# Performance work log

Measured on AMD Instinct MI355X. Metric: run time of the kernel, lower is better.

## Reference

```python
import jax, jax.numpy as jnp
import numpy as np

# Module constants derived from init_kwargs
XYZ_MIN = np.array([-40.0, -40.0, -1.0], dtype=np.float32)
XYZ_MAX = np.array([40.0, 40.0, 5.4], dtype=np.float32)
STEPSIZE = 0.5
VOX = (200, 200, 16)
NUM_VOXELS = VOX[0] * VOX[1] * VOX[2]
VOXEL_SIZE = float((np.prod(XYZ_MAX - XYZ_MIN) / NUM_VOXELS) ** (1.0 / 3.0))  # = 0.4
N_SAMPLES = int(np.linalg.norm(np.array([VOX[0] // 2, VOX[1] // 2, VOX[2] // 2]) + 1) / STEPSIZE) + 1  # 287


def setup_inputs() -> dict:
    key = jax.random.key(0)
    k1, k2, k3 = jax.random.split(key, 3)
    rays_o = jax.random.uniform(k1, (6, 90, 160, 3), dtype=jnp.float32)   # camera origins near scene center
    rays_d = jax.random.normal(k2, (6, 90, 160, 3), dtype=jnp.float32)    # ray directions
    voxel = jax.random.normal(k3, (1, 200, 200, 16), dtype=jnp.float32)   # density grid (C=1, X, Y, Z)
    return {"rays_o": rays_o, "rays_d": rays_d, "voxel": voxel}


def trilinear_sample(grid, pts):
    """align_corners=True trilinear interpolation.
    grid: (C, Dx, Dy, Dz) laid out as (world-x, world-y, world-z) axes
    pts:  (M, 3) world coords. Out-of-range pts are clamped (they are masked later).
    Returns (C, M).
    """
    xyz_min = jnp.asarray(XYZ_MIN)
    xyz_max = jnp.asarray(XYZ_MAX)
    sizes = jnp.asarray(np.array(grid.shape[1:], dtype=np.float32))
    u = (pts - xyz_min) / (xyz_max - xyz_min)              # normalized [0,1]
    idx = jnp.clip(u * (sizes - 1.0), 0.0, sizes - 1.0)    # voxel-space coords
    i0 = jnp.clip(jnp.floor(idx), 0.0, sizes - 2.0).astype(jnp.int32)
    f = idx - i0.astype(idx.dtype)                          # fractional offsets
    x0, y0, z0 = i0[:, 0], i0[:, 1], i0[:, 2]
    fx, fy, fz = f[:, 0], f[:, 1], f[:, 2]
    out = jnp.zeros((grid.shape[0], pts.shape[0]), dtype=grid.dtype)
    for dx in (0, 1):
        wx = fx if dx else (1.0 - fx)
        for dy in (0, 1):
            wy = fy if dy else (1.0 - fy)
            for dz in (0, 1):
                wz = fz if dz else (1.0 - fz)
                corner = grid[:, x0 + dx, y0 + dy, z0 + dz]   # (C, M) gather
                out = out + corner * (wx * wy * wz)[None, :]
    return out


def reference(rays_o, rays_d, voxel):
    xyz_min = jnp.asarray(XYZ_MIN)
    xyz_max = jnp.asarray(XYZ_MAX)
    ro = rays_o.reshape(-1, 3)                                # (M, 3)
    rd = rays_d.reshape(-1, 3)                                # (M, 3)
    # eval-mode sampling: deterministic Zval shared by all rays
    zval = STEPSIZE * VOXEL_SIZE * jnp.arange(N_SAMPLES, dtype=jnp.float32)  # (N,)
    pts = ro[:, None, :] + rd[:, None, :] * zval[None, :, None]             # (M, N, 3)
    mask_out = jnp.any((pts < xyz_min) | (pts > xyz_max), axis=-1)          # (M, N)
    density = trilinear_sample(voxel, pts.reshape(-1, 3))                   # (1, M*N)
    density = density.reshape(pts.shape[0], N_SAMPLES)                      # (M, N)
    # alpha compositing (render_type='density')
    delta = zval[-1] - zval[-2]                                             # constant step length
    alpha = jnp.where(mask_out, 0.0, 1.0 - jnp.exp(-jax.nn.softplus(density) * delta))
    trans = jnp.cumprod(jnp.clip(1.0 - alpha, 1e-10, None), axis=-1)        # (M, N)
    alphainv_cum = jnp.concatenate([jnp.ones_like(trans[:, :1]), trans], axis=-1)
    weights = alpha * alphainv_cum[:, :-1]                                  # (M, N)
    depth = jnp.sum(weights * zval[None, :], axis=-1)                       # (M,)
    return depth
```

## Files before the change

kernel.cpp:

```cpp
#include <hip/hip_runtime.h>
#include <math.h>

#define N_RAYS 86400
#define N_SAMP 287
#define GRP_W  16
#define N_CHUNK 18
#define LOG2E 1.4426950408889634f

#define ROW_SHR_OLD1(x, N)                                                   \
    __int_as_float(__builtin_amdgcn_update_dpp(                              \
        0x3f800000 , __float_as_int(x), 0x110 | (N), 0xF, 0xF, false))

#define SWZ(x, pat) __int_as_float(__builtin_amdgcn_ds_swizzle(__float_as_int(x), (pat)))
#define SWZ_BCAST15 0x1F0
#define SWZ_XOR(m)  (((m) << 10) | 0x1F)

struct F2 { float lo, hi; };

__global__ __launch_bounds__(256) void nerf_depth_kernel(
    const float* __restrict__ rays_o,
    const float* __restrict__ rays_d,
    const float* __restrict__ voxel,
    float* __restrict__ depth_out,
    float stepf, float delta)
{
    const int lane = threadIdx.x & 63;
    const int sub  = lane & (GRP_W - 1);
    const int grp  = lane >> 4;
    const int wave = (blockIdx.x * blockDim.x + threadIdx.x) >> 6;
    const int ray  = wave * 4 + grp;

    const float ox = rays_o[3*ray+0], oy = rays_o[3*ray+1], oz = rays_o[3*ray+2];
    const float dx = rays_d[3*ray+0], dy = rays_d[3*ray+1], dz = rays_d[3*ray+2];

    const float cx1 = 199.0f / 80.0f;                  const float cx0 = 40.0f * cx1;
    const float cz1 = 15.0f / (5.4f - (-1.0f));        const float cz0 = 1.0f * cz1;
    const float negdelta = -delta;

    float T = 1.0f;
    float depth_acc = 0.0f;
    bool  done = false;

    for (int c = 0; c < N_CHUNK; ++c) {
        const int  s     = c * GRP_W + sub;
        const bool valid = (s < N_SAMP);
        const float z  = __fmul_rn(stepf, (float)s);
        const float px = __fadd_rn(ox, __fmul_rn(dx, z));
        const float py = __fadd_rn(oy, __fmul_rn(dy, z));
        const float pz = __fadd_rn(oz, __fmul_rn(dz, z));
        const bool inside = !((fmaxf(fabsf(px), fabsf(py)) > 40.0f) |
                              (pz < -1.0f) | (pz > 5.4f));
        const bool inb = (!done) && valid && inside;

        const unsigned long long bal = __ballot(inb);
        if (((unsigned)(bal >> (grp * GRP_W)) & 0xFFFFu) == 0u) done = true;
        if (__all(done)) break;

        float alpha = 0.0f, az = 0.0f;
        if (inb) {
            float ix = fminf(fmaxf(__builtin_fmaf(px, cx1, cx0), 0.0f), 199.0f);
            float iy = fminf(fmaxf(__builtin_fmaf(py, cx1, cx0), 0.0f), 199.0f);
            float iz = fminf(fmaxf(__builtin_fmaf(pz, cz1, cz0), 0.0f), 15.0f);
            int x0 = min((int)ix, 198);
            int y0 = min((int)iy, 198);
            int z0 = min((int)iz, 14);
            float fx = ix - (float)x0;
            float fy = iy - (float)y0;
            float fz = iz - (float)z0;
            const float* p00 = voxel + ((x0 * 200 + y0) * 16 + z0);
            F2 q00, q01, q10, q11;
            __builtin_memcpy(&q00, p00,        8);
            __builtin_memcpy(&q01, p00 + 16,   8);
            __builtin_memcpy(&q10, p00 + 3200, 8);
            __builtin_memcpy(&q11, p00 + 3216, 8);
            float c00 = q00.lo + fz * (q00.hi - q00.lo);
            float c01 = q01.lo + fz * (q01.hi - q01.lo);
            float c10 = q10.lo + fz * (q10.hi - q10.lo);
            float c11 = q11.lo + fz * (q11.hi - q11.lo);
            float c0  = c00 + fy * (c01 - c00);
            float c1  = c10 + fy * (c11 - c10);
            float d   = c0  + fx * (c1  - c0);
            float e2 = exp2f(d * LOG2E);
            float lg = __log2f(1.0f + e2);
            alpha = 1.0f - exp2f(negdelta * lg);
            az = alpha * z;
        }

        float g = fmaxf(1.0f - alpha, 1e-10f);

        float P = g;
        P *= ROW_SHR_OLD1(P, 1);
        P *= ROW_SHR_OLD1(P, 2);
        P *= ROW_SHR_OLD1(P, 4);
        P *= ROW_SHR_OLD1(P, 8);
        float E = ROW_SHR_OLD1(P, 1);

        depth_acc = __builtin_fmaf(az, T * E, depth_acc);
        T *= SWZ(P, SWZ_BCAST15);

        if (T < 1e-6f) done = true;
    }

    depth_acc += SWZ(depth_acc, SWZ_XOR(1));
    depth_acc += SWZ(depth_acc, SWZ_XOR(2));
    depth_acc += SWZ(depth_acc, SWZ_XOR(4));
    depth_acc += SWZ(depth_acc, SWZ_XOR(8));
    if (sub == 0) depth_out[ray] = depth_acc;
}

extern "C" void kernel_launch(void* const* d_in, const int* in_sizes, int n_in,
                              void* d_out, int out_size, void* d_ws, size_t ws_size,
                              hipStream_t stream) {
    (void)in_sizes; (void)n_in; (void)d_ws; (void)ws_size; (void)out_size;
    const float* rays_o = (const float*)d_in[0];
    const float* rays_d = (const float*)d_in[1];
    const float* voxel  = (const float*)d_in[2];
    float* out = (float*)d_out;

    float rngz  = 5.4f - (-1.0f);
    float prod  = (80.0f * 80.0f) * rngz;
    float ratio = prod / 640000.0f;
    float stepf = (float)(0.5 * pow((double)ratio, 1.0 / 3.0));
    float delta = stepf * 286.0f - stepf * 285.0f;

    nerf_depth_kernel<<<N_RAYS / 16, 256, 0, stream>>>(rays_o, rays_d, voxel, out, stepf, delta);
}
```

Baseline: 26.91 us.

## Sort rays by analytic chunk count to balance wavefront work

Adds two pre-pass kernels. The first computes each ray's exit sample analytically from a ray/box intersection and builds a histogram of chunk counts. The second counting-sorts the rays by that count so rays of similar length share a wavefront, and the main kernel loops only up to each ray's chunk count instead of using a per-chunk ballot. This targets divergence and idle lanes from mixed ray lengths, at the cost of a memset, two extra launches, and scattered ray and output accesses.

```diff
diff --git a/kernel.cpp b/kernel.cpp
--- a/kernel.cpp
+++ b/kernel.cpp
@@ -17,18 +17,80 @@
 
 struct F2 { float lo, hi; };
 
+__device__ __forceinline__ int ray_nch(float ox, float oy, float oz,
+                                       float dx, float dy, float dz,
+                                       float stepf) {
+    float invx = 1.0f / __fmul_rn(dx, stepf);
+    float invy = 1.0f / __fmul_rn(dy, stepf);
+    float invz = 1.0f / __fmul_rn(dz, stepf);
+    float tx = fmaxf((40.0f - ox) * invx, (-40.0f - ox) * invx);
+    float ty = fmaxf((40.0f - oy) * invy, (-40.0f - oy) * invy);
+    float tz = fmaxf((5.4f - oz) * invz, (-1.0f - oz) * invz);
+    float te = fminf(fminf(fminf(tx, ty), tz), 300.0f);
+    int s_stop = min((int)te + 2, N_SAMP);
+    return (s_stop + GRP_W - 1) >> 4;
+}
+
+__global__ __launch_bounds__(256) void k_len(
+    const float* __restrict__ ro, const float* __restrict__ rd,
+    int* __restrict__ nch_arr, int* __restrict__ hist, float stepf)
+{
+    __shared__ int lh[N_CHUNK];
+    if (threadIdx.x < N_CHUNK) lh[threadIdx.x] = 0;
+    __syncthreads();
+    int t = blockIdx.x * 256 + threadIdx.x;
+    if (t < N_RAYS) {
+        int nch = ray_nch(ro[3*t], ro[3*t+1], ro[3*t+2],
+                          rd[3*t], rd[3*t+1], rd[3*t+2], stepf);
+        nch_arr[t] = nch;
+        atomicAdd(&lh[N_CHUNK - nch], 1);
+    }
+    __syncthreads();
+    if (threadIdx.x < N_CHUNK && lh[threadIdx.x])
+        atomicAdd(&hist[threadIdx.x], lh[threadIdx.x]);
+}
+
+__global__ __launch_bounds__(256) void k_scatter(
+    const int* __restrict__ nch_arr, const int* __restrict__ hist,
+    int* __restrict__ cursor, unsigned* __restrict__ sorted)
+{
+    __shared__ int lcount[N_CHUNK], lbase[N_CHUNK];
+    if (threadIdx.x < N_CHUNK) lcount[threadIdx.x] = 0;
+    __syncthreads();
+    int t = blockIdx.x * 256 + threadIdx.x;
+    int b = 0, rank = 0, nch = 0;
+    if (t < N_RAYS) {
+        nch = nch_arr[t];
+        b = N_CHUNK - nch;
+        rank = atomicAdd(&lcount[b], 1);
+    }
+    __syncthreads();
+    if (threadIdx.x < N_CHUNK && lcount[threadIdx.x])
+        lbase[threadIdx.x] = atomicAdd(&cursor[threadIdx.x], lcount[threadIdx.x]);
+    __syncthreads();
+    if (t < N_RAYS) {
+        int off = 0;
+        #pragma unroll
+        for (int i = 0; i < N_CHUNK; ++i) off += (i < b) ? hist[i] : 0;
+        sorted[off + lbase[b] + rank] = (unsigned)t | ((unsigned)nch << 20);
+    }
+}
+
 __global__ __launch_bounds__(256) void nerf_depth_kernel(
     const float* __restrict__ rays_o,
     const float* __restrict__ rays_d,
     const float* __restrict__ voxel,
+    const unsigned* __restrict__ sorted,
     float* __restrict__ depth_out,
     float stepf, float delta)
 {
     const int lane = threadIdx.x & 63;
     const int sub  = lane & (GRP_W - 1);
-    const int grp  = lane >> 4;
-    const int wave = (blockIdx.x * blockDim.x + threadIdx.x) >> 6;
-    const int ray  = wave * 4 + grp;
+    const int g    = (blockIdx.x * blockDim.x + threadIdx.x) >> 4;
+
+    const unsigned e = sorted[g];
+    const int ray = e & 0xFFFFF;
+    const int nch = e >> 20;
 
     const float ox = rays_o[3*ray+0], oy = rays_o[3*ray+1], oz = rays_o[3*ray+2];
     const float dx = rays_d[3*ray+0], dy = rays_d[3*ray+1], dz = rays_d[3*ray+2];
@@ -39,9 +101,10 @@
 
     float T = 1.0f;
     float depth_acc = 0.0f;
-    bool  done = false;
+    bool  dead = false;
 
-    for (int c = 0; c < N_CHUNK; ++c) {
+    int c = 0;
+    while (true) {
         const int  s     = c * GRP_W + sub;
         const bool valid = (s < N_SAMP);
         const float z  = __fmul_rn(stepf, (float)s);
@@ -50,11 +113,7 @@
         const float pz = __fadd_rn(oz, __fmul_rn(dz, z));
         const bool inside = !((fmaxf(fabsf(px), fabsf(py)) > 40.0f) |
                               (pz < -1.0f) | (pz > 5.4f));
-        const bool inb = (!done) && valid && inside;
-
-        const unsigned long long bal = __ballot(inb);
-        if (((unsigned)(bal >> (grp * GRP_W)) & 0xFFFFu) == 0u) done = true;
-        if (__all(done)) break;
+        const bool inb = inside && valid && !dead;
 
         float alpha = 0.0f, az = 0.0f;
         if (inb) {
@@ -86,9 +145,9 @@
             az = alpha * z;
         }
 
-        float g = fmaxf(1.0f - alpha, 1e-10f);
+        float gg = fmaxf(1.0f - alpha, 1e-10f);
 
-        float P = g;
+        float P = gg;
         P *= ROW_SHR_OLD1(P, 1);
         P *= ROW_SHR_OLD1(P, 2);
         P *= ROW_SHR_OLD1(P, 4);
@@ -98,7 +157,9 @@
         depth_acc = __builtin_fmaf(az, T * E, depth_acc);
         T *= SWZ(P, SWZ_BCAST15);
 
-        if (T < 1e-6f) done = true;
+        ++c;
+        dead = dead | (c >= nch) | (T < 1e-6f);
+        if (__all(dead)) break;
     }
 
     depth_acc += SWZ(depth_acc, SWZ_XOR(1));
@@ -111,11 +172,16 @@
 extern "C" void kernel_launch(void* const* d_in, const int* in_sizes, int n_in,
                               void* d_out, int out_size, void* d_ws, size_t ws_size,
                               hipStream_t stream) {
-    (void)in_sizes; (void)n_in; (void)d_ws; (void)ws_size; (void)out_size;
+    (void)in_sizes; (void)n_in; (void)ws_size; (void)out_size;
     const float* rays_o = (const float*)d_in[0];
     const float* rays_d = (const float*)d_in[1];
     const float* voxel  = (const float*)d_in[2];
     float* out = (float*)d_out;
+
+    int*      hist    = (int*)d_ws;
+    int*      cursor  = (int*)d_ws + 32;
+    int*      nch_arr = (int*)d_ws + 1024;
+    unsigned* sorted  = (unsigned*)((int*)d_ws + 1024 + N_RAYS);
 
     float rngz  = 5.4f - (-1.0f);
     float prod  = (80.0f * 80.0f) * rngz;
@@ -123,5 +189,10 @@
     float stepf = (float)(0.5 * pow((double)ratio, 1.0 / 3.0));
     float delta = stepf * 286.0f - stepf * 285.0f;
 
-    nerf_depth_kernel<<<N_RAYS / 16, 256, 0, stream>>>(rays_o, rays_d, voxel, out, stepf, delta);
+    hipMemsetAsync(d_ws, 0, 256, stream);
+    const int pb = (N_RAYS + 255) / 256;
+    k_len    <<<pb, 256, 0, stream>>>(rays_o, rays_d, nch_arr, hist, stepf);
+    k_scatter<<<pb, 256, 0, stream>>>(nch_arr, hist, cursor, sorted);
+    nerf_depth_kernel<<<N_RAYS / 16, 256, 0, stream>>>(rays_o, rays_d, voxel,
+                                                       sorted, out, stepf, delta);
 }
```

Result: slower. 38.92 us (+44.6%).

## Reformulate depth as telescoping transmittance sum and precompute ray exit chunk

Applied to the files above, without the earlier changes.

Rewrites depth compositing algebraically: instead of accumulating alpha*z*T per sample, it accumulates the inclusive transmittance prefix and recovers depth as stepf*(sum - 16*C*U). The per-chunk ballot is replaced by an analytic ray/box exit computation, and the gather/interpolation runs unconditionally with masking done by a select. Swizzles are replaced with DPP quad-perm and row-rotate reductions. Together these aim to cut cross-lane latency and divergence. In exchange, out-of-box lanes now issue loads and transcendentals, the 1e-10 clamp is dropped, and the telescoped form may round differently.

```diff
diff --git a/kernel.cpp b/kernel.cpp
--- a/kernel.cpp
+++ b/kernel.cpp
@@ -7,13 +7,14 @@
 #define N_CHUNK 18
 #define LOG2E 1.4426950408889634f
 
-#define ROW_SHR_OLD1(x, N)                                                   \
-    __int_as_float(__builtin_amdgcn_update_dpp(                              \
-        0x3f800000 , __float_as_int(x), 0x110 | (N), 0xF, 0xF, false))
-
-#define SWZ(x, pat) __int_as_float(__builtin_amdgcn_ds_swizzle(__float_as_int(x), (pat)))
-#define SWZ_BCAST15 0x1F0
-#define SWZ_XOR(m)  (((m) << 10) | 0x1F)
+#define DPP(x, ctrl) __int_as_float(__builtin_amdgcn_update_dpp(             \
+        0, __float_as_int(x), (ctrl), 0xF, 0xF, false))
+#define ROW_SHR_OLD1(x, N) __int_as_float(__builtin_amdgcn_update_dpp(       \
+        0x3f800000, __float_as_int(x), 0x110 | (N), 0xF, 0xF, false))
+#define QPERM_X1 0xB1
+#define QPERM_X2 0x4E
+#define ROW_ROR4 0x124
+#define ROW_ROR8 0x128
 
 struct F2 { float lo, hi; };
 
@@ -33,79 +34,90 @@
     const float ox = rays_o[3*ray+0], oy = rays_o[3*ray+1], oz = rays_o[3*ray+2];
     const float dx = rays_d[3*ray+0], dy = rays_d[3*ray+1], dz = rays_d[3*ray+2];
 
-    const float cx1 = 199.0f / 80.0f;                  const float cx0 = 40.0f * cx1;
-    const float cz1 = 15.0f / (5.4f - (-1.0f));        const float cz0 = 1.0f * cz1;
+    const float cx1 = 199.0f / 80.0f;              const float cx0 = 40.0f * cx1;
+    const float cz1 = 15.0f / (5.4f - (-1.0f));    const float cz0 = 1.0f * cz1;
     const float negdelta = -delta;
 
-    float T = 1.0f;
-    float depth_acc = 0.0f;
-    bool  done = false;
+    int nch;
+    {
+        float ivx = 1.0f / __fmul_rn(dx, stepf);
+        float ivy = 1.0f / __fmul_rn(dy, stepf);
+        float ivz = 1.0f / __fmul_rn(dz, stepf);
+        float tx = fmaxf((40.0f - ox) * ivx, (-40.0f - ox) * ivx);
+        float ty = fmaxf((40.0f - oy) * ivy, (-40.0f - oy) * ivy);
+        float tz = fmaxf((5.4f - oz) * ivz, (-1.0f - oz) * ivz);
+        float te = fminf(fminf(fminf(tx, ty), tz), 300.0f);
+        int s_stop = min((int)te + 2, N_SAMP);
+        nch = (s_stop + GRP_W - 1) >> 4;
+    }
+
+    float U   = 1.0f;
+    float acc = 0.0f;
+    int   C   = 0;
 
     for (int c = 0; c < N_CHUNK; ++c) {
-        const int  s     = c * GRP_W + sub;
-        const bool valid = (s < N_SAMP);
+        const int   s  = c * GRP_W + sub;
         const float z  = __fmul_rn(stepf, (float)s);
         const float px = __fadd_rn(ox, __fmul_rn(dx, z));
         const float py = __fadd_rn(oy, __fmul_rn(dy, z));
         const float pz = __fadd_rn(oz, __fmul_rn(dz, z));
-        const bool inside = !((fmaxf(fabsf(px), fabsf(py)) > 40.0f) |
-                              (pz < -1.0f) | (pz > 5.4f));
-        const bool inb = (!done) && valid && inside;
+        const bool inb = !((fmaxf(fabsf(px), fabsf(py)) > 40.0f) |
+                           (pz < -1.0f) | (pz > 5.4f)) && (s < N_SAMP);
 
-        const unsigned long long bal = __ballot(inb);
-        if (((unsigned)(bal >> (grp * GRP_W)) & 0xFFFFu) == 0u) done = true;
-        if (__all(done)) break;
+        float ix = fminf(fmaxf(__builtin_fmaf(px, cx1, cx0), 0.0f), 199.0f);
+        float iy = fminf(fmaxf(__builtin_fmaf(py, cx1, cx0), 0.0f), 199.0f);
+        float iz = fminf(fmaxf(__builtin_fmaf(pz, cz1, cz0), 0.0f), 15.0f);
+        int x0 = min((int)ix, 198);
+        int y0 = min((int)iy, 198);
+        int z0 = min((int)iz, 14);
+        float fx = ix - (float)x0;
+        float fy = iy - (float)y0;
+        float fz = iz - (float)z0;
+        const float* p00 = voxel + ((x0 * 200 + y0) * 16 + z0);
+        F2 q00, q01, q10, q11;
+        __builtin_memcpy(&q00, p00,        8);
+        __builtin_memcpy(&q01, p00 + 16,   8);
+        __builtin_memcpy(&q10, p00 + 3200, 8);
+        __builtin_memcpy(&q11, p00 + 3216, 8);
+        float c00 = q00.lo + fz * (q00.hi - q00.lo);
+        float c01 = q01.lo + fz * (q01.hi - q01.lo);
+        float c10 = q10.lo + fz * (q10.hi - q10.lo);
+        float c11 = q11.lo + fz * (q11.hi - q11.lo);
+        float c0  = c00 + fy * (c01 - c00);
+        float c1  = c10 + fy * (c11 - c10);
+        float d   = c0  + fx * (c1  - c0);
 
-        float alpha = 0.0f, az = 0.0f;
-        if (inb) {
-            float ix = fminf(fmaxf(__builtin_fmaf(px, cx1, cx0), 0.0f), 199.0f);
-            float iy = fminf(fmaxf(__builtin_fmaf(py, cx1, cx0), 0.0f), 199.0f);
-            float iz = fminf(fmaxf(__builtin_fmaf(pz, cz1, cz0), 0.0f), 15.0f);
-            int x0 = min((int)ix, 198);
-            int y0 = min((int)iy, 198);
-            int z0 = min((int)iz, 14);
-            float fx = ix - (float)x0;
-            float fy = iy - (float)y0;
-            float fz = iz - (float)z0;
-            const float* p00 = voxel + ((x0 * 200 + y0) * 16 + z0);
-            F2 q00, q01, q10, q11;
-            __builtin_memcpy(&q00, p00,        8);
-            __builtin_memcpy(&q01, p00 + 16,   8);
-            __builtin_memcpy(&q10, p00 + 3200, 8);
-            __builtin_memcpy(&q11, p00 + 3216, 8);
-            float c00 = q00.lo + fz * (q00.hi - q00.lo);
-            float c01 = q01.lo + fz * (q01.hi - q01.lo);
-            float c10 = q10.lo + fz * (q10.hi - q10.lo);
-            float c11 = q11.lo + fz * (q11.hi - q11.lo);
-            float c0  = c00 + fy * (c01 - c00);
-            float c1  = c10 + fy * (c11 - c10);
-            float d   = c0  + fx * (c1  - c0);
-            float e2 = exp2f(d * LOG2E);
-            float lg = __log2f(1.0f + e2);
-            alpha = 1.0f - exp2f(negdelta * lg);
-            az = alpha * z;
-        }
-
-        float g = fmaxf(1.0f - alpha, 1e-10f);
+        float e2 = exp2f(d * LOG2E);
+        float lg = __log2f(1.0f + e2);
+        float g  = exp2f(negdelta * lg);
+        g = inb ? g : 1.0f;
 
         float P = g;
         P *= ROW_SHR_OLD1(P, 1);
         P *= ROW_SHR_OLD1(P, 2);
         P *= ROW_SHR_OLD1(P, 4);
         P *= ROW_SHR_OLD1(P, 8);
-        float E = ROW_SHR_OLD1(P, 1);
+        float rho = g;
+        rho *= DPP(rho, QPERM_X1);
+        rho *= DPP(rho, QPERM_X2);
+        rho *= DPP(rho, ROW_ROR4);
+        rho *= DPP(rho, ROW_ROR8);
 
-        depth_acc = __builtin_fmaf(az, T * E, depth_acc);
-        T *= SWZ(P, SWZ_BCAST15);
+        acc = __builtin_fmaf(U, P, acc);
+        U *= rho;
+        C = c + 1;
 
-        if (T < 1e-6f) done = true;
+        const bool dead = (U < 1e-6f) | (C >= nch);
+        if (__all(dead)) break;
     }
 
-    depth_acc += SWZ(depth_acc, SWZ_XOR(1));
-    depth_acc += SWZ(depth_acc, SWZ_XOR(2));
-    depth_acc += SWZ(depth_acc, SWZ_XOR(4));
-    depth_acc += SWZ(depth_acc, SWZ_XOR(8));
-    if (sub == 0) depth_out[ray] = depth_acc;
+    float asum = acc;
+    asum += DPP(asum, QPERM_X1);
+    asum += DPP(asum, QPERM_X2);
+    asum += DPP(asum, ROW_ROR4);
+    asum += DPP(asum, ROW_ROR8);
+    if (sub == 0)
+        depth_out[ray] = stepf * (asum - (float)(GRP_W * C) * U);
 }
 
 extern "C" void kernel_launch(void* const* d_in, const int* in_sizes, int n_in,
@@ -123,5 +135,6 @@
     float stepf = (float)(0.5 * pow((double)ratio, 1.0 / 3.0));
     float delta = stepf * 286.0f - stepf * 285.0f;
 
-    nerf_depth_kernel<<<N_RAYS / 16, 256, 0, stream>>>(rays_o, rays_d, voxel, out, stepf, delta);
+    nerf_depth_kernel<<<N_RAYS / 16, 256, 0, stream>>>(rays_o, rays_d, voxel,
+                                                       out, stepf, delta);
 }
```

Result: slower. 34.72 us (+29.0%).

## Pack voxel z-pairs into half2 workspace to halve gather bytes

Applied to the files above, without the earlier changes.

Adds a pre-pass kernel that converts the float voxel grid into a half2 array holding each cell's value and its +z neighbour. The main kernel then gathers four 4-byte half2 values instead of four 8-byte float pairs, so gather traffic and cache footprint are halved and each load is aligned. In exchange it adds a second kernel launch plus a full read and write of the grid every call, and fp16 storage loses precision in the density values.

```diff
diff --git a/kernel.cpp b/kernel.cpp
--- a/kernel.cpp
+++ b/kernel.cpp
@@ -1,4 +1,5 @@
 #include <hip/hip_runtime.h>
+#include <hip/hip_fp16.h>
 #include <math.h>
 
 #define N_RAYS 86400
@@ -6,6 +7,7 @@
 #define GRP_W  16
 #define N_CHUNK 18
 #define LOG2E 1.4426950408889634f
+#define N_CELLS (200 * 200 * 16)
 
 #define ROW_SHR_OLD1(x, N)                                                   \
     __int_as_float(__builtin_amdgcn_update_dpp(                              \
@@ -15,12 +17,21 @@
 #define SWZ_BCAST15 0x1F0
 #define SWZ_XOR(m)  (((m) << 10) | 0x1F)
 
-struct F2 { float lo, hi; };
+__global__ __launch_bounds__(256) void pack_zpair_kernel(
+    const float* __restrict__ v, __half2* __restrict__ zp)
+{
+    int idx = blockIdx.x * blockDim.x + threadIdx.x;
+    if (idx >= N_CELLS) return;
+    int z  = idx & 15;
+    float a = v[idx];
+    float b = (z < 15) ? v[idx + 1] : a;
+    zp[idx] = __floats2half2_rn(a, b);
+}
 
 __global__ __launch_bounds__(256) void nerf_depth_kernel(
     const float* __restrict__ rays_o,
     const float* __restrict__ rays_d,
-    const float* __restrict__ voxel,
+    const __half2* __restrict__ zp,
     float* __restrict__ depth_out,
     float stepf, float delta)
 {
@@ -67,16 +78,15 @@
             float fx = ix - (float)x0;
             float fy = iy - (float)y0;
             float fz = iz - (float)z0;
-            const float* p00 = voxel + ((x0 * 200 + y0) * 16 + z0);
-            F2 q00, q01, q10, q11;
-            __builtin_memcpy(&q00, p00,        8);
-            __builtin_memcpy(&q01, p00 + 16,   8);
-            __builtin_memcpy(&q10, p00 + 3200, 8);
-            __builtin_memcpy(&q11, p00 + 3216, 8);
-            float c00 = q00.lo + fz * (q00.hi - q00.lo);
-            float c01 = q01.lo + fz * (q01.hi - q01.lo);
-            float c10 = q10.lo + fz * (q10.hi - q10.lo);
-            float c11 = q11.lo + fz * (q11.hi - q11.lo);
+            const int cell = (x0 * 200 + y0) * 16 + z0;
+            __half2 h00 = zp[cell];
+            __half2 h01 = zp[cell + 16];
+            __half2 h10 = zp[cell + 3200];
+            __half2 h11 = zp[cell + 3216];
+            float c00 = __low2float(h00) + fz * (__high2float(h00) - __low2float(h00));
+            float c01 = __low2float(h01) + fz * (__high2float(h01) - __low2float(h01));
+            float c10 = __low2float(h10) + fz * (__high2float(h10) - __low2float(h10));
+            float c11 = __low2float(h11) + fz * (__high2float(h11) - __low2float(h11));
             float c0  = c00 + fy * (c01 - c00);
             float c1  = c10 + fy * (c11 - c10);
             float d   = c0  + fx * (c1  - c0);
@@ -111,11 +121,12 @@
 extern "C" void kernel_launch(void* const* d_in, const int* in_sizes, int n_in,
                               void* d_out, int out_size, void* d_ws, size_t ws_size,
                               hipStream_t stream) {
-    (void)in_sizes; (void)n_in; (void)d_ws; (void)ws_size; (void)out_size;
+    (void)in_sizes; (void)n_in; (void)ws_size; (void)out_size;
     const float* rays_o = (const float*)d_in[0];
     const float* rays_d = (const float*)d_in[1];
     const float* voxel  = (const float*)d_in[2];
     float* out = (float*)d_out;
+    __half2* zp = (__half2*)d_ws;
 
     float rngz  = 5.4f - (-1.0f);
     float prod  = (80.0f * 80.0f) * rngz;
@@ -123,5 +134,7 @@
     float stepf = (float)(0.5 * pow((double)ratio, 1.0 / 3.0));
     float delta = stepf * 286.0f - stepf * 285.0f;
 
-    nerf_depth_kernel<<<N_RAYS / 16, 256, 0, stream>>>(rays_o, rays_d, voxel, out, stepf, delta);
+    pack_zpair_kernel<<<(N_CELLS + 255) / 256, 256, 0, stream>>>(voxel, zp);
+    nerf_depth_kernel<<<N_RAYS / 16, 256, 0, stream>>>(rays_o, rays_d, zp,
+                                                       out, stepf, delta);
 }
```

Result: slower. 32.62 us (+21.2%).
